# Kernel optimization log

Measured on AMD Instinct MI355X. Metric: run time of the kernel, lower is better.

## Reference

```python
import jax, jax.numpy as jnp
import numpy as np

DIM = 1536; HEADS = 12; HD = DIM // HEADS; FFN = 8960; EPS = 1e-6; T5 = 512
B = 1; F_ = 8; H_ = 18; W_ = 24; S = F_ * H_ * W_; L2 = T5 + 257


def _ln(x, w=None, b=None):
    m = x.mean(-1, keepdims=True)
    v = ((x - m) ** 2).mean(-1, keepdims=True)
    y = (x - m) * jax.lax.rsqrt(v + EPS)
    return y * w + b if w is not None else y


def _rms(x, w):
    return x * jax.lax.rsqrt(jnp.mean(x * x, -1, keepdims=True) + EPS) * w


def _gelu_tanh(z):
    return 0.5 * z * (1.0 + jnp.tanh(0.7978845608028654 * (z + 0.044715 * z * z * z)))


def _rope(x, F, H, W, ang):
    # x: [B,S,n,d]; ang: [1024, d//2] rotation angles (axial 3D RoPE)
    b, s, n, d = x.shape
    c = d // 2
    c1 = c // 3; c0 = c - 2 * c1  # split sizes [c0, c1, c1] over (F,H,W)
    fa = jnp.broadcast_to(ang[:F, :c0][:, None, None, :], (F, H, W, c0))
    ha = jnp.broadcast_to(ang[:H, c0:c0 + c1][None, :, None, :], (F, H, W, c1))
    wa = jnp.broadcast_to(ang[:W, c0 + c1:][None, None, :, :], (F, H, W, c1))
    th = jnp.concatenate([fa, ha, wa], -1).reshape(1, s, 1, c)
    cs, sn = jnp.cos(th), jnp.sin(th)
    xr = x.reshape(b, s, n, c, 2)
    re, im = xr[..., 0], xr[..., 1]
    return jnp.stack([re * cs - im * sn, re * sn + im * cs], -1).reshape(b, s, n, d)


def _attn(q, k, v):
    # dense softmax attention; [B,Lq,n,d] x [B,Lk,n,d]
    s = jnp.einsum('bqnd,bknd->bnqk', q, k) * (1.0 / np.sqrt(q.shape[-1]))
    p = jax.nn.softmax(s, axis=-1)
    return jnp.einsum('bnqk,bknd->bqnd', p, v)


def setup_inputs() -> dict:
    key = jax.random.key(0)
    ks = iter(jax.random.split(key, 64))
    g = lambda shp, sc=0.02: jax.random.normal(next(ks), shp, dtype=jnp.float32) * sc
    inp = {
        'x': jax.random.normal(next(ks), (B, S, DIM), dtype=jnp.float32),
        'e': jax.random.normal(next(ks), (B, 6, DIM), dtype=jnp.float32),
        'context': jax.random.normal(next(ks), (B, L2, DIM), dtype=jnp.float32),
        'freqs': jax.random.uniform(next(ks), (1024, HD // 2), dtype=jnp.float32),
        'modulation': g((1, 6, DIM)),
        'sa_qw': g((DIM, DIM)), 'sa_qb': jnp.zeros((DIM,), jnp.float32),
        'sa_kw': g((DIM, DIM)), 'sa_kb': jnp.zeros((DIM,), jnp.float32),
        'sa_vw': g((DIM, DIM)), 'sa_vb': jnp.zeros((DIM,), jnp.float32),
        'sa_ow': g((DIM, DIM)), 'sa_ob': jnp.zeros((DIM,), jnp.float32),
        'sa_nq': jnp.ones((DIM,), jnp.float32), 'sa_nk': jnp.ones((DIM,), jnp.float32),
        'norm3_w': jnp.ones((DIM,), jnp.float32), 'norm3_b': jnp.zeros((DIM,), jnp.float32),
        'ca_qw': g((DIM, DIM)), 'ca_qb': jnp.zeros((DIM,), jnp.float32),
        'ca_kw': g((DIM, DIM)), 'ca_kb': jnp.zeros((DIM,), jnp.float32),
        'ca_vw': g((DIM, DIM)), 'ca_vb': jnp.zeros((DIM,), jnp.float32),
        'ca_kiw': g((DIM, DIM)), 'ca_kib': jnp.zeros((DIM,), jnp.float32),
        'ca_viw': g((DIM, DIM)), 'ca_vib': jnp.zeros((DIM,), jnp.float32),
        'ca_ow': g((DIM, DIM)), 'ca_ob': jnp.zeros((DIM,), jnp.float32),
        'ca_nq': jnp.ones((DIM,), jnp.float32), 'ca_nk': jnp.ones((DIM,), jnp.float32),
        'ca_nki': jnp.ones((DIM,), jnp.float32),
        'ffn_w1': g((DIM, FFN)), 'ffn_b1': jnp.zeros((FFN,), jnp.float32),
        'ffn_w2': g((FFN, DIM)), 'ffn_b2': jnp.zeros((DIM,), jnp.float32),
        'F': F_, 'H': H_, 'W': W_,
    }
    return inp


def reference(x, e, context, freqs, modulation, sa_qw, sa_qb, sa_kw, sa_kb, sa_vw, sa_vb,
              sa_ow, sa_ob, sa_nq, sa_nk, norm3_w, norm3_b, ca_qw, ca_qb, ca_kw, ca_kb,
              ca_vw, ca_vb, ca_kiw, ca_kib, ca_viw, ca_vib, ca_ow, ca_ob, ca_nq, ca_nk,
              ca_nki, ffn_w1, ffn_b1, ffn_w2, ffn_b2, F, H, W):
    b, s, c = x.shape
    e6 = modulation + e                    # [B,6,C]
    e0, e1, e2, e3, e4, e5 = [e6[:, i:i + 1] for i in range(6)]

    # ---- self attention (with 3D RoPE, qk RMSNorm) ----
    xs = _ln(x) * (1.0 + e1) + e0
    q = _rms(xs @ sa_qw + sa_qb, sa_nq).reshape(b, s, HEADS, HD)
    k = _rms(xs @ sa_kw + sa_kb, sa_nk).reshape(b, s, HEADS, HD)
    v = (xs @ sa_vw + sa_vb).reshape(b, s, HEADS, HD)
    q = _rope(q, F, H, W, freqs)
    k = _rope(k, F, H, W, freqs)
    y = _attn(q, k, v).reshape(b, s, c) @ sa_ow + sa_ob
    x = x + y * e2

    # ---- i2v cross attention: text tokens (last T5) + image tokens (first L2-T5) ----
    xc = _ln(x, norm3_w, norm3_b)
    img_len = context.shape[1] - T5
    ctx_img = context[:, :img_len]
    ctx_txt = context[:, img_len:]
    q = _rms(xc @ ca_qw + ca_qb, ca_nq).reshape(b, s, HEADS, HD)
    k = _rms(ctx_txt @ ca_kw + ca_kb, ca_nk).reshape(b, T5, HEADS, HD)
    v = (ctx_txt @ ca_vw + ca_vb).reshape(b, T5, HEADS, HD)
    ki = _rms(ctx_img @ ca_kiw + ca_kib, ca_nki).reshape(b, img_len, HEADS, HD)
    vi = (ctx_img @ ca_viw + ca_vib).reshape(b, img_len, HEADS, HD)
    a = _attn(q, k, v) + _attn(q, ki, vi)
    x = x + a.reshape(b, s, c) @ ca_ow + ca_ob

    # ---- FFN with adaLN modulation ----
    z = _ln(x) * (1.0 + e4) + e3
    y = _gelu_tanh(z @ ffn_w1 + ffn_b1) @ ffn_w2 + ffn_b2
    x = x + y * e5
    return x
```

## Files before the change

kernel.cpp:

```cpp
#include <hip/hip_runtime.h>
#include <stdint.h>

#define DIM 1536
#define NHEADS 12
#define HD 128
#define FFN 8960
#define SQ 3456
#define T5 512
#define LCTX 769
#define IMG 257
#define IMGP 384
#define EPSL 1e-6f

typedef __bf16 bf16;
typedef __bf16 bf16x8 __attribute__((ext_vector_type(8)));
typedef float f32x4 __attribute__((ext_vector_type(4)));

__device__ inline bf16x8 zero_bf16x8() {
  bf16x8 v;
  for (int i = 0; i < 8; i++) v[i] = (bf16)0.0f;
  return v;
}

__device__ inline void glds16(const bf16* g, bf16* lds) {
  __builtin_amdgcn_global_load_lds(
      (const __attribute__((address_space(1))) void*)g,
      (__attribute__((address_space(3))) void*)lds, 16, 0, 0);
}

__device__ inline bf16x8 rot8(bf16x8 v, int r) {
  union U { bf16x8 b; uint32_t d[4]; };
  U u; u.b = v;
  uint32_t e0 = (r & 4) ? u.d[2] : u.d[0], e1 = (r & 4) ? u.d[3] : u.d[1];
  uint32_t e2 = (r & 4) ? u.d[0] : u.d[2], e3 = (r & 4) ? u.d[1] : u.d[3];
  uint32_t f0 = (r & 2) ? e1 : e0, f1 = (r & 2) ? e2 : e1;
  uint32_t f2 = (r & 2) ? e3 : e2, f3 = (r & 2) ? e0 : e3;
  U o;
  o.d[0] = (r & 1) ? __builtin_amdgcn_alignbit(f1, f0, 16) : f0;
  o.d[1] = (r & 1) ? __builtin_amdgcn_alignbit(f2, f1, 16) : f1;
  o.d[2] = (r & 1) ? __builtin_amdgcn_alignbit(f3, f2, 16) : f2;
  o.d[3] = (r & 1) ? __builtin_amdgcn_alignbit(f0, f3, 16) : f3;
  return o.b;
}


__global__ void prep_small_kernel(const float* __restrict__ modv, const float* __restrict__ e,
                                  float* __restrict__ e6f,
                                  const float* __restrict__ qb, const float* __restrict__ kb,
                                  const float* __restrict__ vb, float* __restrict__ qkvB,
                                  const float* __restrict__ ckb, const float* __restrict__ cvb,
                                  float* __restrict__ kvB,
                                  const float* __restrict__ kib, const float* __restrict__ vib,
                                  float* __restrict__ kivB) {
  int i = blockIdx.x * 256 + threadIdx.x;
  if (i < 6 * DIM) e6f[i] = modv[i] + e[i];
  if (i < DIM) {
    qkvB[i] = qb[i]; qkvB[i + DIM] = kb[i]; qkvB[i + 2 * DIM] = vb[i];
    kvB[i] = ckb[i]; kvB[i + DIM] = cvb[i];
    kivB[i] = kib[i]; kivB[i + DIM] = vib[i];
  }
}

__global__ void prep_ctx_kernel(const float* __restrict__ ctx, bf16* __restrict__ ctxt,
                                bf16* __restrict__ ctxi) {
  int i = blockIdx.x * 256 + threadIdx.x;
  if (i < T5 * DIM) ctxt[i] = (bf16)ctx[(size_t)IMG * DIM + i];
  if (i < IMGP * DIM) {
    int r = i / DIM;
    ctxi[i] = (r < IMG) ? (bf16)ctx[i] : (bf16)0.0f;
  }
}

__global__ void transpose_w3_kernel(const float* __restrict__ W0, const float* __restrict__ W1,
                                    const float* __restrict__ W2, bf16* __restrict__ Wt,
                                    int K, int N) {
  __shared__ float tile[32][33];
  const float* W = blockIdx.z == 0 ? W0 : (blockIdx.z == 1 ? W1 : W2);
  bf16* dst = Wt + (size_t)blockIdx.z * K * N;
  int n0 = blockIdx.x * 32, k0 = blockIdx.y * 32;
  int tx = threadIdx.x, ty = threadIdx.y;
  for (int i = ty; i < 32; i += 8)
    tile[i][tx] = W[(size_t)(k0 + i) * N + n0 + tx];
  __syncthreads();
  for (int i = ty; i < 32; i += 8)
    dst[(size_t)(n0 + i) * K + k0 + tx] = (bf16)tile[tx][i];
}

__device__ inline void block_reduce2(float& s1, float& s2) {
  __shared__ float buf[8];
  for (int off = 32; off; off >>= 1) {
    s1 += __shfl_down(s1, off, 64);
    s2 += __shfl_down(s2, off, 64);
  }
  int w = threadIdx.x >> 6;
  if ((threadIdx.x & 63) == 0) { buf[w] = s1; buf[w + 4] = s2; }
  __syncthreads();
  s1 = buf[0] + buf[1] + buf[2] + buf[3];
  s2 = buf[4] + buf[5] + buf[6] + buf[7];
  __syncthreads();
}

__global__ __launch_bounds__(256) void ln_mod_kernel(
    const float* __restrict__ X, const float* __restrict__ gamma,
    const float* __restrict__ beta, int plus_one, bf16* __restrict__ out) {
  int r = blockIdx.x;
  const float* xr = X + (size_t)r * DIM;
  float v[6], s = 0.f, s2 = 0.f;
  for (int i = 0; i < 6; i++) {
    v[i] = xr[threadIdx.x + i * 256];
    s += v[i]; s2 += v[i] * v[i];
  }
  block_reduce2(s, s2);
  float mean = s * (1.0f / DIM);
  float var = s2 * (1.0f / DIM) - mean * mean;
  float rstd = rsqrtf(var + EPSL);
  float add1 = plus_one ? 1.0f : 0.0f;
  for (int i = 0; i < 6; i++) {
    int c = threadIdx.x + i * 256;
    out[(size_t)r * DIM + c] = (bf16)(((v[i] - mean) * rstd) * (gamma[c] + add1) + beta[c]);
  }
}

__global__ __launch_bounds__(256) void rms_rope_multi_kernel(
    const float* __restrict__ X, int istride, int nsec,
    const float* __restrict__ nw0, const float* __restrict__ nw1,
    int mode0, int mode1, int mode2,
    const float* __restrict__ freqs,
    bf16* __restrict__ o0, bf16* __restrict__ o1, bf16* __restrict__ o2) {
  int sec = blockIdx.y;
  int r = blockIdx.x;
  const float* xr = X + (size_t)r * istride + sec * DIM;
  const float* nw = sec == 0 ? nw0 : nw1;
  bf16* out = (sec == 0 ? o0 : (sec == 1 ? o1 : o2)) + (size_t)r * DIM;
  int mode = sec == 0 ? mode0 : (sec == 1 ? mode1 : mode2);
  float v[6];
  for (int i = 0; i < 6; i++) v[i] = xr[threadIdx.x + i * 256];
  if (mode == 0) {
    for (int i = 0; i < 6; i++) out[threadIdx.x + i * 256] = (bf16)v[i];
    return;
  }
  float s2 = 0.f, dummy = 0.f;
  for (int i = 0; i < 6; i++) s2 += v[i] * v[i];
  block_reduce2(s2, dummy);
  float rms = rsqrtf(s2 * (1.0f / DIM) + EPSL);
  if (mode == 1) {
    for (int i = 0; i < 6; i++) {
      int c = threadIdx.x + i * 256;
      out[c] = (bf16)(v[i] * rms * nw[c]);
    }
  } else {
    int f = r / (18 * 24), rem = r % (18 * 24), hh = rem / 24, ww = rem % 24;
    for (int i = 0; i < 3; i++) {
      int p = threadIdx.x + i * 256;
      int id = p & 63;
      int idx = id < 22 ? f : (id < 43 ? hh : ww);
      float th = freqs[idx * 64 + id];
      float cs = __cosf(th), sn = __sinf(th);
      float re = xr[2 * p] * rms * nw[2 * p];
      float im = xr[2 * p + 1] * rms * nw[2 * p + 1];
      out[2 * p]     = (bf16)(re * cs - im * sn);
      out[2 * p + 1] = (bf16)(re * sn + im * cs);
    }
  }
}

__global__ void ffn2_reduce_kernel(const float* __restrict__ p, const float* __restrict__ b2,
                                   const float* __restrict__ e5, const float* __restrict__ xcur,
                                   float* __restrict__ out) {
  int i = blockIdx.x * 256 + threadIdx.x;
  if (i >= SQ * DIM) return;
  int col = i % DIM;
  out[i] = xcur[i] + (p[i] + p[i + (size_t)SQ * DIM] + b2[col]) * e5[col];
}

template <int BM>
__global__ __launch_bounds__(256) void gemm_db_kernel(
    const bf16* __restrict__ A, const bf16* __restrict__ Wt,
    const float* __restrict__ bias, const float* __restrict__ scalev,
    const float* __restrict__ resid, float* __restrict__ outF,
    bf16* __restrict__ outB, int M, int N, int K, int gelu, int ksplit) {
  constexpr int MI = BM / 32;
  constexpr int NAW = BM / 64;
  __shared__ bf16 As[2][BM * 32];
  __shared__ bf16 Bs[2][128 * 32];
  int tid = threadIdx.x;
  int tm0 = blockIdx.y * BM, tn0 = blockIdx.x * 128;
  int lane = tid & 63, wave = tid >> 6;
  int quad = lane >> 4, l16 = lane & 15;
  int mbase = (wave >> 1) * (BM / 2), nbase = (wave & 1) * 64;
  int lrow = lane >> 2, lcol = (lane & 3) * 8;
  int klen = K / ksplit;
  int kbeg = blockIdx.z * klen;

  const bf16* aP[NAW];
  const bf16* bP[2];
#pragma unroll
  for (int j = 0; j < NAW; j++) {
    int c = wave * NAW + j;
    aP[j] = A + (size_t)(tm0 + c * 16 + lrow) * K + kbeg + lcol;
  }
#pragma unroll
  for (int j = 0; j < 2; j++) {
    int c = wave * 2 + j;
    bP[j] = Wt + (size_t)(tn0 + c * 16 + lrow) * K + kbeg + lcol;
  }

  f32x4 acc[MI][4];
#pragma unroll
  for (int mi = 0; mi < MI; mi++)
    for (int ni = 0; ni < 4; ni++)
      for (int rr = 0; rr < 4; rr++) acc[mi][ni][rr] = 0.0f;

  auto stage = [&](int buf) {
#pragma unroll
    for (int j = 0; j < NAW; j++) {
      glds16(aP[j], &As[buf][(wave * NAW + j) * 512]);
      aP[j] += 32;
    }
#pragma unroll
    for (int j = 0; j < 2; j++) {
      glds16(bP[j], &Bs[buf][(wave * 2 + j) * 512]);
      bP[j] += 32;
    }
  };

  int niter = klen / 32;
  stage(0);
  int cur = 0;
  for (int it = 0; it < niter; it++) {
    __syncthreads();
    if (it + 1 < niter) stage(cur ^ 1);
    bf16x8 af[MI], bfr[4];
#pragma unroll
    for (int mi = 0; mi < MI; mi++)
      af[mi] = *(bf16x8*)&As[cur][(mbase + mi * 16 + l16) * 32 + quad * 8];
#pragma unroll
    for (int ni = 0; ni < 4; ni++)
      bfr[ni] = *(bf16x8*)&Bs[cur][(nbase + ni * 16 + l16) * 32 + quad * 8];
#pragma unroll
    for (int mi = 0; mi < MI; mi++)
#pragma unroll
      for (int ni = 0; ni < 4; ni++)
        acc[mi][ni] = __builtin_amdgcn_mfma_f32_16x16x32_bf16(af[mi], bfr[ni], acc[mi][ni], 0, 0, 0);
    cur ^= 1;
  }

  if (ksplit > 1) {
    float* po = outF + (size_t)blockIdx.z * M * N;
#pragma unroll
    for (int mi = 0; mi < MI; mi++) {
      int rbase = tm0 + mbase + mi * 16 + quad * 4;
#pragma unroll
      for (int ni = 0; ni < 4; ni++) {
        int col = tn0 + nbase + ni * 16 + l16;
        for (int rr = 0; rr < 4; rr++)
          po[(size_t)(rbase + rr) * N + col] = acc[mi][ni][rr];
      }
    }
    return;
  }

#pragma unroll
  for (int mi = 0; mi < MI; mi++) {
    int rbase = tm0 + mbase + mi * 16 + quad * 4;
#pragma unroll
    for (int ni = 0; ni < 4; ni++) {
      int col = tn0 + nbase + ni * 16 + l16;
      float b = bias ? bias[col] : 0.0f;
      float sc = scalev ? scalev[col] : 1.0f;
      for (int rr = 0; rr < 4; rr++) {
        int row = rbase + rr;
        float t = acc[mi][ni][rr] + b;
        if (gelu) {
          float z = t;
          float u = 0.7978845608028654f * (z + 0.044715f * z * z * z);
          t = z / (1.0f + __expf(-2.0f * u));
        }
        t *= sc;
        size_t idx = (size_t)row * N + col;
        if (resid) t += resid[idx];
        if (outF) outF[idx] = t;
        else outB[idx] = (bf16)t;
      }
    }
  }
}

__global__ __launch_bounds__(256) void attn_kernel(
    const bf16* __restrict__ Q, const bf16* __restrict__ Kb, const bf16* __restrict__ Vb,
    float* __restrict__ Opart, float* __restrict__ mlb,
    int L, int kchunk, int zoff) {
  __shared__ bf16 Ks[32][136];
  __shared__ bf16 Vts[128][40];
  __shared__ bf16 Ps[4][16][40];

  int nwg = gridDim.x * gridDim.y * gridDim.z;
  int flat = blockIdx.x + gridDim.x * (blockIdx.y + gridDim.y * blockIdx.z);
  if ((nwg & 7) == 0) flat = (flat & 7) * (nwg >> 3) + (flat >> 3);
  int bx = flat % gridDim.x;
  int rest = flat / gridDim.x;
  int hb = rest % gridDim.y;
  int bz = rest / gridDim.y;

  int tid = threadIdx.x;
  int q0 = bx * 64;
  int zabs = zoff + bz;
  int kbeg = bz * kchunk;
  int kend = min(L, kbeg + kchunk);
  int klen = kend - kbeg;
  int lane = tid & 63, wave = tid >> 6;
  int quad = lane >> 4, l16 = lane & 15;
  int qrow = q0 + wave * 16 + l16;

  bf16x8 qf[4];
#pragma unroll
  for (int c = 0; c < 4; c++)
    qf[c] = *(const bf16x8*)(Q + (size_t)qrow * DIM + hb * HD + c * 32 + quad * 8);

  f32x4 o[8];
#pragma unroll
  for (int ff = 0; ff < 8; ff++)
    for (int rr = 0; rr < 4; rr++) o[ff][rr] = 0.0f;
  float m_i[4], l_i[4];
#pragma unroll
  for (int r = 0; r < 4; r++) { m_i[r] = -1e30f; l_i[r] = 0.0f; }
  const float sc = 0.08838834764831845f;

  int srow = tid >> 3, scolc = tid & 7, scol = scolc * 16;
  int nt = (klen + 31) / 32;

  const bf16* kp0 = Kb + (size_t)(kbeg + srow) * DIM + hb * HD + scol;
  const bf16* vp0 = Vb + (size_t)(kbeg + srow) * DIM + hb * HD + scol;

  bf16x8 k0v, k1v, v0v, v1v;
  if (srow < klen) {
    k0v = *(const bf16x8*)kp0; k1v = *(const bf16x8*)(kp0 + 8);
    v0v = *(const bf16x8*)vp0; v1v = *(const bf16x8*)(vp0 + 8);
  } else {
    k0v = zero_bf16x8(); k1v = zero_bf16x8();
    v0v = zero_bf16x8(); v1v = zero_bf16x8();
  }

  for (int kt = 0; kt < nt; kt++) {
    __syncthreads();
    *(bf16x8*)&Ks[srow][scol] = k0v;
    *(bf16x8*)&Ks[srow][scol + 8] = k1v;
    {
      bf16x8 r0 = rot8(v0v, scolc), r1 = rot8(v1v, scolc);
#pragma unroll
      for (int i = 0; i < 8; i++) {
        int jj = (i + scolc) & 7;
        Vts[scol + jj][srow] = r0[i];
        Vts[scol + 8 + jj][srow] = r1[i];
      }
    }
    if (kt + 1 < nt) {
      int key = (kt + 1) * 32 + srow;
      const bf16* kp = kp0 + (size_t)(kt + 1) * 32 * DIM;
      const bf16* vp = vp0 + (size_t)(kt + 1) * 32 * DIM;
      if (key < klen) {
        k0v = *(const bf16x8*)kp; k1v = *(const bf16x8*)(kp + 8);
        v0v = *(const bf16x8*)vp; v1v = *(const bf16x8*)(vp + 8);
      } else {
        k0v = zero_bf16x8(); k1v = zero_bf16x8();
        v0v = zero_bf16x8(); v1v = zero_bf16x8();
      }
    }
    __syncthreads();

    f32x4 sfr[2];
    __builtin_amdgcn_s_setprio(1);
#pragma unroll
    for (int nf = 0; nf < 2; nf++) {
      f32x4 a;
      for (int rr = 0; rr < 4; rr++) a[rr] = 0.0f;
#pragma unroll
      for (int c = 0; c < 4; c++) {
        bf16x8 kf = *(bf16x8*)&Ks[nf * 16 + l16][c * 32 + quad * 8];
        a = __builtin_amdgcn_mfma_f32_16x16x32_bf16(qf[c], kf, a, 0, 0, 0);
      }
      sfr[nf] = a;
    }
    __builtin_amdgcn_s_setprio(0);

#pragma unroll
    for (int nf = 0; nf < 2; nf++) {
      int colg = kt * 32 + nf * 16 + l16;
      bool valid = colg < klen;
#pragma unroll
      for (int r = 0; r < 4; r++)
        sfr[nf][r] = valid ? sfr[nf][r] * sc : -1e30f;
    }
    float mnew[4], alpha[4];
#pragma unroll
    for (int r = 0; r < 4; r++) {
      float t = fmaxf(sfr[0][r], sfr[1][r]);
#pragma unroll
      for (int off = 1; off < 16; off <<= 1) t = fmaxf(t, __shfl_xor(t, off, 64));
      mnew[r] = fmaxf(m_i[r], t);
      alpha[r] = __expf(m_i[r] - mnew[r]);
      m_i[r] = mnew[r];
    }
#pragma unroll
    for (int r = 0; r < 4; r++) {
      float p0 = __expf(sfr[0][r] - mnew[r]);
      float p1 = __expf(sfr[1][r] - mnew[r]);
      char* prow = (char*)&Ps[wave][quad * 4 + r][0];
      *(bf16*)(prow + ((l16 * 2) ^ (quad << 4))) = (bf16)p0;
      *(bf16*)(prow + ((32 + l16 * 2) ^ (quad << 4))) = (bf16)p1;
      float t = p0 + p1;
#pragma unroll
      for (int off = 1; off < 16; off <<= 1) t += __shfl_xor(t, off, 64);
      l_i[r] = l_i[r] * alpha[r] + t;
#pragma unroll
      for (int ff = 0; ff < 8; ff++) o[ff][r] *= alpha[r];
    }
    bf16x8 pf = *(bf16x8*)((char*)&Ps[wave][l16][0] + ((quad * 16) ^ ((l16 >> 2) << 4)));
    __builtin_amdgcn_s_setprio(1);
#pragma unroll
    for (int ff = 0; ff < 8; ff++) {
      bf16x8 vf = *(bf16x8*)&Vts[ff * 16 + l16][quad * 8];
      o[ff] = __builtin_amdgcn_mfma_f32_16x16x32_bf16(pf, vf, o[ff], 0, 0, 0);
    }
    __builtin_amdgcn_s_setprio(0);
  }

  float* po = Opart + (size_t)zabs * SQ * DIM;
#pragma unroll
  for (int r = 0; r < 4; r++) {
    float inv = 1.0f / l_i[r];
#pragma unroll
    for (int ff = 0; ff < 8; ff++) o[ff][r] *= inv;
  }
#pragma unroll
  for (int ff = 0; ff < 8; ff++) {
#pragma unroll
    for (int r = 0; r < 4; r++) {
      int row = q0 + wave * 16 + quad * 4 + r;
      int col = hb * HD + ff * 16 + l16;
      po[(size_t)row * DIM + col] = o[ff][r];
    }
  }
  if (l16 == 0) {
#pragma unroll
    for (int r = 0; r < 4; r++) {
      int row = q0 + wave * 16 + quad * 4 + r;
      size_t mi = (((size_t)zabs * NHEADS + hb) * SQ + row) * 2;
      mlb[mi] = m_i[r];
      mlb[mi + 1] = l_i[r];
    }
  }
}

__global__ __launch_bounds__(256) void attn_combine_kernel(
    const float* __restrict__ Op, const float* __restrict__ mlb,
    bf16* __restrict__ out, int nmerge, int addslot) {
  int row = blockIdx.x;
  __shared__ float wsh[3 * NHEADS];
  int t = threadIdx.x;
  if (t < NHEADS) {
    float m[3], l[3];
    for (int z = 0; z < 3; z++) {
      if (z < nmerge) {
        size_t b = (((size_t)z * NHEADS + t) * SQ + row) * 2;
        m[z] = mlb[b]; l[z] = mlb[b + 1];
      } else {
        m[z] = -1e30f; l[z] = 0.0f;
      }
    }
    float M = fmaxf(m[0], fmaxf(m[1], m[2]));
    float w0 = l[0] * __expf(m[0] - M);
    float w1 = l[1] * __expf(m[1] - M);
    float w2 = l[2] * __expf(m[2] - M);
    float inv = 1.0f / (w0 + w1 + w2);
    wsh[t] = w0 * inv;
    wsh[NHEADS + t] = w1 * inv;
    wsh[2 * NHEADS + t] = w2 * inv;
  }
  __syncthreads();
#pragma unroll
  for (int i = 0; i < 6; i++) {
    int c = t + i * 256;
    int h = c >> 7;
    float acc = wsh[h] * Op[((size_t)0 * SQ + row) * DIM + c];
    if (nmerge > 1) acc += wsh[NHEADS + h] * Op[((size_t)1 * SQ + row) * DIM + c];
    if (nmerge > 2) acc += wsh[2 * NHEADS + h] * Op[((size_t)2 * SQ + row) * DIM + c];
    if (addslot >= 0) acc += Op[((size_t)addslot * SQ + row) * DIM + c];
    out[(size_t)row * DIM + c] = (bf16)acc;
  }
}


extern "C" void kernel_launch(void* const* d_in, const int* in_sizes, int n_in,
                              void* d_out, int out_size, void* d_ws, size_t ws_size,
                              hipStream_t stream) {
  const float* x      = (const float*)d_in[0];
  const float* e      = (const float*)d_in[1];
  const float* ctx    = (const float*)d_in[2];
  const float* freqs  = (const float*)d_in[3];
  const float* modv   = (const float*)d_in[4];
  const float* sa_qw  = (const float*)d_in[5];
  const float* sa_qb  = (const float*)d_in[6];
  const float* sa_kw  = (const float*)d_in[7];
  const float* sa_kb  = (const float*)d_in[8];
  const float* sa_vw  = (const float*)d_in[9];
  const float* sa_vb  = (const float*)d_in[10];
  const float* sa_ow  = (const float*)d_in[11];
  const float* sa_ob  = (const float*)d_in[12];
  const float* sa_nq  = (const float*)d_in[13];
  const float* sa_nk  = (const float*)d_in[14];
  const float* norm3w = (const float*)d_in[15];
  const float* norm3b = (const float*)d_in[16];
  const float* ca_qw  = (const float*)d_in[17];
  const float* ca_qb  = (const float*)d_in[18];
  const float* ca_kw  = (const float*)d_in[19];
  const float* ca_kb  = (const float*)d_in[20];
  const float* ca_vw  = (const float*)d_in[21];
  const float* ca_vb  = (const float*)d_in[22];
  const float* ca_kiw = (const float*)d_in[23];
  const float* ca_kib = (const float*)d_in[24];
  const float* ca_viw = (const float*)d_in[25];
  const float* ca_vib = (const float*)d_in[26];
  const float* ca_ow  = (const float*)d_in[27];
  const float* ca_ob  = (const float*)d_in[28];
  const float* ca_nq  = (const float*)d_in[29];
  const float* ca_nk  = (const float*)d_in[30];
  const float* ca_nki = (const float*)d_in[31];
  const float* ffn_w1 = (const float*)d_in[32];
  const float* ffn_b1 = (const float*)d_in[33];
  const float* ffn_w2 = (const float*)d_in[34];
  const float* ffn_b2 = (const float*)d_in[35];

  char* ws = (char*)d_ws;
  size_t off = 0;
  auto alloc = [&](size_t bytes) -> void* {
    void* p = ws + off;
    off += (bytes + 255) & ~(size_t)255;
    return p;
  };
  float* e6f   = (float*)alloc((size_t)6 * DIM * 4);
  bf16* act_bf = (bf16*)alloc((size_t)SQ * DIM * 2);
  bf16* q_bf   = (bf16*)alloc((size_t)SQ * DIM * 2);
  bf16* k_bf   = (bf16*)alloc((size_t)SQ * DIM * 2);
  bf16* v_bf   = (bf16*)alloc((size_t)SQ * DIM * 2);
  char* big0   = (char*)alloc((size_t)SQ * 3 * DIM * 4);
  float* xcur  = (float*)alloc((size_t)SQ * DIM * 4);
  bf16* wbig   = (bf16*)alloc((size_t)FFN * DIM * 2);
  bf16* wsm    = (bf16*)alloc((size_t)3 * DIM * DIM * 2);
  bf16* ctxt_bf = (bf16*)alloc((size_t)T5 * DIM * 2);
  bf16* ctxi_bf = (bf16*)alloc((size_t)IMGP * DIM * 2);
  float* ctxkvF = (float*)alloc((size_t)T5 * 2 * DIM * 4);
  float* ctxkivF = (float*)alloc((size_t)IMGP * 2 * DIM * 4);
  bf16* kt_bf  = (bf16*)alloc((size_t)T5 * DIM * 2);
  bf16* vt_bf  = (bf16*)alloc((size_t)T5 * DIM * 2);
  bf16* ki_bf  = (bf16*)alloc((size_t)IMGP * DIM * 2);
  bf16* vi_bf  = (bf16*)alloc((size_t)IMGP * DIM * 2);
  float* qkvB  = (float*)alloc((size_t)3 * DIM * 4);
  float* kvB   = (float*)alloc((size_t)2 * DIM * 4);
  float* kivB  = (float*)alloc((size_t)2 * DIM * 4);
  float* mlbuf = (float*)alloc((size_t)3 * NHEADS * SQ * 2 * 4);

  float* qkvF = (float*)big0;
  float* projf = (float*)big0;
  float* opart = (float*)big0;
  bf16* y1 = (bf16*)big0;
  float* pbuf = (float*)act_bf;

  const float* e0 = e6f;
  const float* e1 = e6f + DIM;
  const float* e2 = e6f + 2 * DIM;
  const float* e3 = e6f + 3 * DIM;
  const float* e4 = e6f + 4 * DIM;
  const float* e5 = e6f + 5 * DIM;

  dim3 tblk(32, 8);

  prep_small_kernel<<<(6 * DIM + 255) / 256, 256, 0, stream>>>(
      modv, e, e6f, sa_qb, sa_kb, sa_vb, qkvB, ca_kb, ca_vb, kvB, ca_kib, ca_vib, kivB);

  ln_mod_kernel<<<SQ, 256, 0, stream>>>(x, e1, e0, 1, act_bf);

  transpose_w3_kernel<<<dim3(48, 48, 3), tblk, 0, stream>>>(sa_qw, sa_kw, sa_vw, wbig, DIM, DIM);
  gemm_db_kernel<128><<<dim3(3 * DIM / 128, SQ / 128), 256, 0, stream>>>(
      act_bf, wbig, qkvB, nullptr, nullptr, qkvF, nullptr, SQ, 3 * DIM, DIM, 0, 1);
  rms_rope_multi_kernel<<<dim3(SQ, 3), 256, 0, stream>>>(
      qkvF, 3 * DIM, 3, sa_nq, sa_nk, 2, 2, 0, freqs, q_bf, k_bf, v_bf);

  attn_kernel<<<dim3(SQ / 64, NHEADS, 3), 256, 0, stream>>>(
      q_bf, k_bf, v_bf, opart, mlbuf, SQ, SQ / 3, 0);
  attn_combine_kernel<<<SQ, 256, 0, stream>>>(opart, mlbuf, act_bf, 3, -1);

  transpose_w3_kernel<<<dim3(48, 48, 1), tblk, 0, stream>>>(sa_ow, nullptr, nullptr, wsm, DIM, DIM);
  gemm_db_kernel<64><<<dim3(DIM / 128, SQ / 64), 256, 0, stream>>>(
      act_bf, wsm, sa_ob, e2, x, xcur, nullptr, SQ, DIM, DIM, 0, 1);

  ln_mod_kernel<<<SQ, 256, 0, stream>>>(xcur, norm3w, norm3b, 0, act_bf);

  transpose_w3_kernel<<<dim3(48, 48, 1), tblk, 0, stream>>>(ca_qw, nullptr, nullptr, wsm, DIM, DIM);
  gemm_db_kernel<64><<<dim3(DIM / 128, SQ / 64), 256, 0, stream>>>(
      act_bf, wsm, ca_qb, nullptr, nullptr, projf, nullptr, SQ, DIM, DIM, 0, 1);
  rms_rope_multi_kernel<<<dim3(SQ, 1), 256, 0, stream>>>(
      projf, DIM, 1, ca_nq, nullptr, 1, 0, 0, freqs, q_bf, nullptr, nullptr);

  prep_ctx_kernel<<<(T5 * DIM + 255) / 256, 256, 0, stream>>>(ctx, ctxt_bf, ctxi_bf);

  transpose_w3_kernel<<<dim3(48, 48, 2), tblk, 0, stream>>>(ca_kw, ca_vw, nullptr, wsm, DIM, DIM);
  gemm_db_kernel<64><<<dim3(2 * DIM / 128, T5 / 64), 256, 0, stream>>>(
      ctxt_bf, wsm, kvB, nullptr, nullptr, ctxkvF, nullptr, T5, 2 * DIM, DIM, 0, 1);
  rms_rope_multi_kernel<<<dim3(T5, 2), 256, 0, stream>>>(
      ctxkvF, 2 * DIM, 2, ca_nk, nullptr, 1, 0, 0, freqs, kt_bf, vt_bf, nullptr);

  transpose_w3_kernel<<<dim3(48, 48, 2), tblk, 0, stream>>>(ca_kiw, ca_viw, nullptr, wsm, DIM, DIM);
  gemm_db_kernel<64><<<dim3(2 * DIM / 128, IMGP / 64), 256, 0, stream>>>(
      ctxi_bf, wsm, kivB, nullptr, nullptr, ctxkivF, nullptr, IMGP, 2 * DIM, DIM, 0, 1);
  rms_rope_multi_kernel<<<dim3(IMGP, 2), 256, 0, stream>>>(
      ctxkivF, 2 * DIM, 2, ca_nki, nullptr, 1, 0, 0, freqs, ki_bf, vi_bf, nullptr);

  attn_kernel<<<dim3(SQ / 64, NHEADS, 2), 256, 0, stream>>>(
      q_bf, kt_bf, vt_bf, opart, mlbuf, T5, T5 / 2, 0);
  attn_kernel<<<dim3(SQ / 64, NHEADS, 1), 256, 0, stream>>>(
      q_bf, ki_bf, vi_bf, opart, mlbuf, IMG, IMG, 2);
  attn_combine_kernel<<<SQ, 256, 0, stream>>>(opart, mlbuf, act_bf, 2, 2);

  transpose_w3_kernel<<<dim3(48, 48, 1), tblk, 0, stream>>>(ca_ow, nullptr, nullptr, wsm, DIM, DIM);
  gemm_db_kernel<64><<<dim3(DIM / 128, SQ / 64), 256, 0, stream>>>(
      act_bf, wsm, ca_ob, nullptr, xcur, xcur, nullptr, SQ, DIM, DIM, 0, 1);

  ln_mod_kernel<<<SQ, 256, 0, stream>>>(xcur, e4, e3, 1, act_bf);

  transpose_w3_kernel<<<dim3(FFN / 32, 48, 1), tblk, 0, stream>>>(ffn_w1, nullptr, nullptr, wbig, DIM, FFN);
  gemm_db_kernel<128><<<dim3(FFN / 128, SQ / 128), 256, 0, stream>>>(
      act_bf, wbig, ffn_b1, nullptr, nullptr, nullptr, y1, SQ, FFN, DIM, 1, 1);

  transpose_w3_kernel<<<dim3(48, FFN / 32, 1), tblk, 0, stream>>>(ffn_w2, nullptr, nullptr, wbig, FFN, DIM);
  gemm_db_kernel<128><<<dim3(DIM / 128, SQ / 128, 2), 256, 0, stream>>>(
      y1, wbig, nullptr, nullptr, nullptr, pbuf, nullptr, SQ, DIM, FFN, 0, 2);
  ffn2_reduce_kernel<<<(SQ * DIM + 255) / 256, 256, 0, stream>>>(
      pbuf, ffn_b2, e5, xcur, (float*)d_out);
}
```

Before: 1.328 ms.

## Widen attention key tile to 64 with lazy rescaling and MFMA row sums

```diff
diff --git a/kernel.cpp b/kernel.cpp
--- a/kernel.cpp
+++ b/kernel.cpp
@@ -290,9 +290,9 @@
     const bf16* __restrict__ Q, const bf16* __restrict__ Kb, const bf16* __restrict__ Vb,
     float* __restrict__ Opart, float* __restrict__ mlb,
     int L, int kchunk, int zoff) {
-  __shared__ bf16 Ks[32][136];
-  __shared__ bf16 Vts[128][40];
-  __shared__ bf16 Ps[4][16][40];
+  __shared__ bf16 Ks[64][136];
+  __shared__ bf16 Vts[128][72];
+  __shared__ bf16 Ps[4][16][72];
 
   int nwg = gridDim.x * gridDim.y * gridDim.z;
   int flat = blockIdx.x + gridDim.x * (blockIdx.y + gridDim.y * blockIdx.z);
@@ -317,6 +317,10 @@
   for (int c = 0; c < 4; c++)
     qf[c] = *(const bf16x8*)(Q + (size_t)qrow * DIM + hb * HD + c * 32 + quad * 8);
 
+  bf16x8 onesv;
+#pragma unroll
+  for (int i = 0; i < 8; i++) onesv[i] = (bf16)1.0f;
+
   f32x4 o[8];
 #pragma unroll
   for (int ff = 0; ff < 8; ff++)
@@ -326,52 +330,61 @@
   for (int r = 0; r < 4; r++) { m_i[r] = -1e30f; l_i[r] = 0.0f; }
   const float sc = 0.08838834764831845f;
 
-  int srow = tid >> 3, scolc = tid & 7, scol = scolc * 16;
-  int nt = (klen + 31) / 32;
-
-  const bf16* kp0 = Kb + (size_t)(kbeg + srow) * DIM + hb * HD + scol;
-  const bf16* vp0 = Vb + (size_t)(kbeg + srow) * DIM + hb * HD + scol;
-
-  bf16x8 k0v, k1v, v0v, v1v;
+  int srow = tid >> 2, scolc = tid & 3;
+  int rot = (2 * scolc + (srow & 1)) & 7;
+  int nt = (klen + 63) / 64;
+
+  const bf16* kp0 = Kb + (size_t)(kbeg + srow) * DIM + hb * HD + scolc * 8;
+  const bf16* vp0 = Vb + (size_t)(kbeg + srow) * DIM + hb * HD + scolc * 8;
+
+  bf16x8 kreg[4], vreg[4];
   if (srow < klen) {
-    k0v = *(const bf16x8*)kp0; k1v = *(const bf16x8*)(kp0 + 8);
-    v0v = *(const bf16x8*)vp0; v1v = *(const bf16x8*)(vp0 + 8);
+#pragma unroll
+    for (int c = 0; c < 4; c++) {
+      kreg[c] = *(const bf16x8*)(kp0 + c * 32);
+      vreg[c] = *(const bf16x8*)(vp0 + c * 32);
+    }
   } else {
-    k0v = zero_bf16x8(); k1v = zero_bf16x8();
-    v0v = zero_bf16x8(); v1v = zero_bf16x8();
+#pragma unroll
+    for (int c = 0; c < 4; c++) { kreg[c] = zero_bf16x8(); vreg[c] = zero_bf16x8(); }
   }
 
   for (int kt = 0; kt < nt; kt++) {
     __syncthreads();
-    *(bf16x8*)&Ks[srow][scol] = k0v;
-    *(bf16x8*)&Ks[srow][scol + 8] = k1v;
-    {
-      bf16x8 r0 = rot8(v0v, scolc), r1 = rot8(v1v, scolc);
+#pragma unroll
+    for (int c = 0; c < 4; c++)
+      *(bf16x8*)&Ks[srow][scolc * 8 + c * 32] = kreg[c];
+#pragma unroll
+    for (int c = 0; c < 4; c++) {
+      bf16x8 rv = rot8(vreg[c], rot);
+      int v0 = scolc * 8 + c * 32;
 #pragma unroll
       for (int i = 0; i < 8; i++) {
-        int jj = (i + scolc) & 7;
-        Vts[scol + jj][srow] = r0[i];
-        Vts[scol + 8 + jj][srow] = r1[i];
+        int jj = (i + rot) & 7;
+        Vts[v0 + jj][srow] = rv[i];
       }
     }
     if (kt + 1 < nt) {
-      int key = (kt + 1) * 32 + srow;
-      const bf16* kp = kp0 + (size_t)(kt + 1) * 32 * DIM;
-      const bf16* vp = vp0 + (size_t)(kt + 1) * 32 * DIM;
+      int key = (kt + 1) * 64 + srow;
+      const bf16* kp = kp0 + (size_t)(kt + 1) * 64 * DIM;
+      const bf16* vp = vp0 + (size_t)(kt + 1) * 64 * DIM;
       if (key < klen) {
-        k0v = *(const bf16x8*)kp; k1v = *(const bf16x8*)(kp + 8);
-        v0v = *(const bf16x8*)vp; v1v = *(const bf16x8*)(vp + 8);
+#pragma unroll
+        for (int c = 0; c < 4; c++) {
+          kreg[c] = *(const bf16x8*)(kp + c * 32);
+          vreg[c] = *(const bf16x8*)(vp + c * 32);
+        }
       } else {
-        k0v = zero_bf16x8(); k1v = zero_bf16x8();
-        v0v = zero_bf16x8(); v1v = zero_bf16x8();
+#pragma unroll
+        for (int c = 0; c < 4; c++) { kreg[c] = zero_bf16x8(); vreg[c] = zero_bf16x8(); }
       }
     }
     __syncthreads();
 
-    f32x4 sfr[2];
+    f32x4 sfr[4];
     __builtin_amdgcn_s_setprio(1);
 #pragma unroll
-    for (int nf = 0; nf < 2; nf++) {
+    for (int nf = 0; nf < 4; nf++) {
       f32x4 a;
       for (int rr = 0; rr < 4; rr++) a[rr] = 0.0f;
 #pragma unroll
@@ -384,45 +397,67 @@
     __builtin_amdgcn_s_setprio(0);
 
 #pragma unroll
-    for (int nf = 0; nf < 2; nf++) {
-      int colg = kt * 32 + nf * 16 + l16;
+    for (int nf = 0; nf < 4; nf++) {
+      int colg = kt * 64 + nf * 16 + l16;
       bool valid = colg < klen;
 #pragma unroll
       for (int r = 0; r < 4; r++)
         sfr[nf][r] = valid ? sfr[nf][r] * sc : -1e30f;
     }
-    float mnew[4], alpha[4];
+
+    float lmax[4];
+#pragma unroll
+    for (int r = 0; r < 4; r++)
+      lmax[r] = fmaxf(fmaxf(sfr[0][r], sfr[1][r]), fmaxf(sfr[2][r], sfr[3][r]));
+    int ok = (lmax[0] <= m_i[0] + 8.0f) & (lmax[1] <= m_i[1] + 8.0f) &
+             (lmax[2] <= m_i[2] + 8.0f) & (lmax[3] <= m_i[3] + 8.0f);
+    if (!__all(ok)) {
+#pragma unroll
+      for (int r = 0; r < 4; r++) {
+        float t = lmax[r];
+#pragma unroll
+        for (int off = 1; off < 16; off <<= 1) t = fmaxf(t, __shfl_xor(t, off, 64));
+        float mnew = fmaxf(m_i[r], t);
+        float alpha = __expf(m_i[r] - mnew);
+        m_i[r] = mnew;
+        l_i[r] *= alpha;
+#pragma unroll
+        for (int ff = 0; ff < 8; ff++) o[ff][r] *= alpha;
+      }
+    }
+
 #pragma unroll
     for (int r = 0; r < 4; r++) {
-      float t = fmaxf(sfr[0][r], sfr[1][r]);
-#pragma unroll
-      for (int off = 1; off < 16; off <<= 1) t = fmaxf(t, __shfl_xor(t, off, 64));
-      mnew[r] = fmaxf(m_i[r], t);
-      alpha[r] = __expf(m_i[r] - mnew[r]);
-      m_i[r] = mnew[r];
-    }
-#pragma unroll
-    for (int r = 0; r < 4; r++) {
-      float p0 = __expf(sfr[0][r] - mnew[r]);
-      float p1 = __expf(sfr[1][r] - mnew[r]);
       char* prow = (char*)&Ps[wave][quad * 4 + r][0];
-      *(bf16*)(prow + ((l16 * 2) ^ (quad << 4))) = (bf16)p0;
-      *(bf16*)(prow + ((32 + l16 * 2) ^ (quad << 4))) = (bf16)p1;
-      float t = p0 + p1;
-#pragma unroll
-      for (int off = 1; off < 16; off <<= 1) t += __shfl_xor(t, off, 64);
-      l_i[r] = l_i[r] * alpha[r] + t;
-#pragma unroll
-      for (int ff = 0; ff < 8; ff++) o[ff][r] *= alpha[r];
-    }
-    bf16x8 pf = *(bf16x8*)((char*)&Ps[wave][l16][0] + ((quad * 16) ^ ((l16 >> 2) << 4)));
+      int swzW = ((quad >> 1) & 1) << 5;
+#pragma unroll
+      for (int nf = 0; nf < 4; nf++) {
+        float p = __expf(sfr[nf][r] - m_i[r]);
+        *(bf16*)(prow + (((nf * 16 + l16) * 2) ^ swzW)) = (bf16)p;
+      }
+    }
+    int swzR = ((l16 >> 3) & 1) << 5;
+    bf16x8 pf[2];
+#pragma unroll
+    for (int ks = 0; ks < 2; ks++)
+      pf[ks] = *(bf16x8*)((char*)&Ps[wave][l16][0] + (((ks * 32 + quad * 8) * 2) ^ swzR));
+
     __builtin_amdgcn_s_setprio(1);
+    f32x4 ld;
+    for (int rr = 0; rr < 4; rr++) ld[rr] = 0.0f;
+    ld = __builtin_amdgcn_mfma_f32_16x16x32_bf16(pf[0], onesv, ld, 0, 0, 0);
+    ld = __builtin_amdgcn_mfma_f32_16x16x32_bf16(pf[1], onesv, ld, 0, 0, 0);
 #pragma unroll
     for (int ff = 0; ff < 8; ff++) {
-      bf16x8 vf = *(bf16x8*)&Vts[ff * 16 + l16][quad * 8];
-      o[ff] = __builtin_amdgcn_mfma_f32_16x16x32_bf16(pf, vf, o[ff], 0, 0, 0);
+#pragma unroll
+      for (int ks = 0; ks < 2; ks++) {
+        bf16x8 vf = *(bf16x8*)&Vts[ff * 16 + l16][ks * 32 + quad * 8];
+        o[ff] = __builtin_amdgcn_mfma_f32_16x16x32_bf16(pf[ks], vf, o[ff], 0, 0, 0);
+      }
     }
     __builtin_amdgcn_s_setprio(0);
+#pragma unroll
+    for (int r = 0; r < 4; r++) l_i[r] += ld[r];
   }
 
   float* po = Opart + (size_t)zabs * SQ * DIM;
```

After: 1.244 ms. 1.07x faster.
